# Kernel optimization log

Hardware: AMD Instinct MI355X
Metric: run time of the kernel (lower is better)

Reference implementation:

```python
import jax, jax.numpy as jnp
import numpy as np

TAU = 2.0       # LIF time constant
ALPHA = 4.0     # spikingjelly Sigmoid surrogate alpha
EPS = 1e-5      # BatchNorm eps
NUM_HEADS = 8

@jax.custom_vjp
def _spike(x):
    return (x >= 0.0).astype(x.dtype)

def _spike_fwd(x):
    return _spike(x), x

def _spike_bwd(x, g):
    s = jax.nn.sigmoid(ALPHA * x)
    return (g * ALPHA * s * (1.0 - s),)

_spike.defvjp(_spike_fwd, _spike_bwd)

def lif(x, v_th=1.0):
    """Multi-step LIF over leading time axis. v <- v + (x - v)/tau; hard reset to 0.
    detach_reset=True: spike in reset path is stop-gradient'ed."""
    def step(v, xt):
        v = v + (xt - v) / TAU
        s = _spike(v - v_th)
        v = v * (1.0 - jax.lax.stop_gradient(s))
        return v, s
    _, out = jax.lax.scan(step, jnp.zeros_like(x[0]), x)
    return out

def conv_bn(x, w, gamma, beta, mean, var, bias=None):
    """1x1 Conv1d over channel dim + BatchNorm1d (inference-style, running stats).
    x: [T,B,C,N], w: [Cout,Cin]."""
    y = jnp.einsum('tbcn,dc->tbdn', x, w)
    if bias is not None:
        y = y + bias[None, None, :, None]
    inv = gamma * jax.lax.rsqrt(var + EPS)
    return (y - mean[None, None, :, None]) * inv[None, None, :, None] + beta[None, None, :, None]

def _bn_params(key, C):
    k1, k2, k3 = jax.random.split(key, 3)
    gamma = 1.0 + 0.1 * jax.random.normal(k1, (C,), jnp.float32)
    beta = 0.1 * jax.random.normal(k2, (C,), jnp.float32)
    mean = 0.1 * jax.random.normal(k3, (C,), jnp.float32)
    var = jnp.ones((C,), jnp.float32)
    return gamma, beta, mean, var

def setup_inputs() -> dict:
    key = jax.random.key(0)
    ks = jax.random.split(key, 10)
    T, B, C, N = 4, 8, 512, 1024
    scale = 1.0 / np.sqrt(C)
    d = {}
    d['q'] = jax.random.normal(ks[0], (T, B, C, N), jnp.float32)
    d['k'] = jax.random.normal(ks[1], (T, B, C, N), jnp.float32)
    d['q_w'] = jax.random.normal(ks[2], (C, C), jnp.float32) * scale
    d['k_w'] = jax.random.normal(ks[3], (C, C), jnp.float32) * scale
    d['proj_w'] = jax.random.normal(ks[4], (C, C), jnp.float32) * scale
    d['proj_b'] = 0.01 * jax.random.normal(ks[5], (C,), jnp.float32)
    d['q_gamma'], d['q_beta'], d['q_mean'], d['q_var'] = _bn_params(ks[6], C)
    d['k_gamma'], d['k_beta'], d['k_mean'], d['k_var'] = _bn_params(ks[7], C)
    d['proj_gamma'], d['proj_beta'], d['proj_mean'], d['proj_var'] = _bn_params(ks[8], C)
    return d

def reference(q, k, q_w, k_w, proj_w, proj_b,
              q_gamma, q_beta, q_mean, q_var,
              k_gamma, k_beta, k_mean, k_var,
              proj_gamma, proj_beta, proj_mean, proj_var):
    T, B, C, N = q.shape
    H = NUM_HEADS
    Dh = C // H
    # Q path: conv1x1 + BN + LIF spikes, split heads
    q_s = lif(conv_bn(q, q_w, q_gamma, q_beta, q_mean, q_var))          # [T,B,C,N]
    q_h = q_s.reshape(T, B, H, Dh, N)
    # K path
    k_s = lif(conv_bn(k, k_w, k_gamma, k_beta, k_mean, k_var))          # [T,B,C,N]
    k_h = k_s.reshape(T, B, H, Dh, N)
    # Sum-pool Q over head_dim, spike-gate (threshold 0.5), multiply into K
    q_sum = jnp.sum(q_h, axis=3, keepdims=True)                         # [T,B,H,1,N]
    attn = lif(q_sum, v_th=0.5)                                         # [T,B,H,1,N]
    x = (attn * k_h).reshape(T, B, C, N)
    # Projection: conv1x1 (with bias) + BN + LIF
    x = conv_bn(x, proj_w, proj_gamma, proj_beta, proj_mean, proj_var, bias=proj_b)
    return lif(x)
```

## Files before the change

kernel.cpp:

```cpp
#include <hip/hip_runtime.h>
#include <hip/hip_fp16.h>
#include <stdint.h>

#define TT 4
#define BB 8
#define CC 512
#define NN 1024
#define HH 8

typedef unsigned char u8;
typedef _Float16 f16x8 __attribute__((ext_vector_type(8)));
typedef float f32x16 __attribute__((ext_vector_type(16)));

#define WF_BYTES ((size_t)2*64*512*16)
#define SZ_SPIKE ((size_t)TT*BB*CC*NN)
#define SZ_GATE  ((size_t)TT*BB*HH*NN)

union U4H { uint4 u; f16x8 v; };
__device__ __forceinline__ f16x8 ash(uint4 u){ U4H x; x.u = u; return x.v; }

#define MFMA_F16(a,b,c) __builtin_amdgcn_mfma_f32_32x32x16_f16((a),(b),(c),0,0,0)

__device__ __forceinline__ void gld_lds4(const void* g, void* l){
  __builtin_amdgcn_global_load_lds((const __attribute__((address_space(1))) void*)g,
                                   (__attribute__((address_space(3))) void*)l, 4, 0, 0);
}

#define WAITVM(N) asm volatile("s_waitcnt vmcnt(" #N ")" ::: "memory")
#define WAITLGKM0 asm volatile("s_waitcnt lgkmcnt(0)" ::: "memory")
#define SBAR() __builtin_amdgcn_s_barrier()
#define VMFENCE() asm volatile("" ::: "memory")

__device__ __forceinline__ void split16(float xs, uint32_t& h, uint32_t& m){
  __half hh = __float2half(xs);
  float hf = __half2float(hh);
  __half mm = __float2half(xs - hf);
  h = __half_as_ushort(hh);
  m = __half_as_ushort(mm);
}

__global__ __launch_bounds__(256)
void k_prep(const float* __restrict__ W0, const float* __restrict__ W1,
            const float* __restrict__ W2,
            u8* __restrict__ D0, u8* __restrict__ D1, u8* __restrict__ D2)
{
  const int which = blockIdx.y;
  const float* W = (which == 0) ? W0 : (which == 1) ? W1 : W2;
  u8* D = (which == 0) ? D0 : (which == 1) ? D1 : D2;
  const int tg  = blockIdx.x * 256 + threadIdx.x;
  const int row = tg >> 6;
  const int kh  = tg & 63;
  uint32_t Hw[4], Mw[4];
#pragma unroll
  for (int p = 0; p < 4; ++p){
    uint32_t h0, m0, h1, m1;
    split16(W[row * CC + kh * 8 + 2*p    ] * 64.0f, h0, m0);
    split16(W[row * CC + kh * 8 + 2*p + 1] * 64.0f, h1, m1);
    Hw[p] = h0 | (h1 << 16);
    Mw[p] = m0 | (m1 << 16);
  }
  *(uint4*)(D + ((size_t)(0*64 + kh)*512 + row) * 16) = make_uint4(Hw[0],Hw[1],Hw[2],Hw[3]);
  *(uint4*)(D + ((size_t)(1*64 + kh)*512 + row) * 16) = make_uint4(Mw[0],Mw[1],Mw[2],Mw[3]);
}

__global__ __launch_bounds__(256, 1)
void k_qk(const float* __restrict__ Q, const float* __restrict__ K,
          const u8* __restrict__ WFq, const u8* __restrict__ WFk,
          const float* __restrict__ qg, const float* __restrict__ qb,
          const float* __restrict__ qm, const float* __restrict__ qv,
          const float* __restrict__ kg, const float* __restrict__ kb,
          const float* __restrict__ km, const float* __restrict__ kv,
          u8* __restrict__ Sk, u8* __restrict__ Aa)
{
  __shared__ uint4 frag[2][1024];

  const int hw = blockIdx.x;
  const int lg = (hw & 7) * 64 + (hw >> 3);
  const int n0i  = lg & 31;
  const int b    = (lg >> 5) & 7;
  const int path = (lg >> 8) & 1;
  const int n0 = n0i << 5;
  const float* X = path ? K : Q;
  const u8* WF = path ? WFk : WFq;

  const int tid = threadIdx.x, lane = tid & 63, wid = tid >> 6;
  const int hi = lane >> 5, ln31 = lane & 31;

  const int c  = tid & 127;
  const int kq = tid >> 7;
  const int ct_t = c >> 5, nn = c & 31;
  const float* Xb = X + ((size_t)(ct_t*BB + b)*CC)*NN + n0 + nn;

  f32x16 acc[4][4];
#pragma unroll
  for (int i = 0; i < 4; ++i)
#pragma unroll
    for (int j = 0; j < 4; ++j)
#pragma unroll
      for (int r = 0; r < 16; ++r) acc[i][j][r] = 0.0f;

  uint4 A[16];
  float xb[2][16];

  auto loadA = [&](int H){
#pragma unroll
    for (int s = 0; s < 2; ++s)
#pragma unroll
      for (int ks = 0; ks < 2; ++ks)
#pragma unroll
        for (int rt = 0; rt < 4; ++rt)
          A[(s*2 + ks)*4 + rt] = *(const uint4*)(WF +
              ((size_t)(s*64 + H*4 + ks*2 + hi)*512
               + wid*128 + rt*32 + ln31) * 16);
  };
  auto loadX = [&](int ktile, float* xr){
    const float* xp = Xb + (size_t)(ktile*32 + kq*16)*NN;
#pragma unroll
    for (int j = 0; j < 16; ++j) xr[j] = xp[(size_t)j*NN];
  };
  auto split_write = [&](const float* xr, int fb){
    uint32_t hw_[8], mw_[8];
#pragma unroll
    for (int p = 0; p < 8; ++p){
      uint32_t ha, ma, hb2, mb2;
      split16(xr[2*p    ] * 512.0f, ha, ma);
      split16(xr[2*p + 1] * 512.0f, hb2, mb2);
      hw_[p] = ha | (hb2 << 16);
      mw_[p] = ma | (mb2 << 16);
    }
    frag[fb][(kq*2    )*128 + c] = make_uint4(hw_[0],hw_[1],hw_[2],hw_[3]);
    frag[fb][(kq*2 + 1)*128 + c] = make_uint4(hw_[4],hw_[5],hw_[6],hw_[7]);
    frag[fb][(4 + kq*2    )*128 + c] = make_uint4(mw_[0],mw_[1],mw_[2],mw_[3]);
    frag[fb][(4 + kq*2 + 1)*128 + c] = make_uint4(mw_[4],mw_[5],mw_[6],mw_[7]);
  };
  auto mstep = [&](int fb){
#pragma unroll
    for (int ks = 0; ks < 2; ++ks){
      const int kbi = ks*2 + hi;
#pragma unroll
      for (int ct = 0; ct < 4; ++ct){
        f16x8 bh = ash(frag[fb][kbi*128 + ct*32 + ln31]);
        f16x8 bm = ash(frag[fb][(4 + kbi)*128 + ct*32 + ln31]);
#pragma unroll
        for (int rt = 0; rt < 4; ++rt){
          acc[ct][rt] = MFMA_F16(ash(A[(0*2 + ks)*4 + rt]), bh, acc[ct][rt]);
          acc[ct][rt] = MFMA_F16(ash(A[(1*2 + ks)*4 + rt]), bh, acc[ct][rt]);
          acc[ct][rt] = MFMA_F16(ash(A[(0*2 + ks)*4 + rt]), bm, acc[ct][rt]);
        }
      }
    }
  };

#define QK_PH(H, XL, XN, FC, FN) { \
    loadA(H); VMFENCE(); \
    loadX((H)+2, xb[XN]); VMFENCE(); \
    split_write(xb[XL], FN); \
    mstep(FC); \
    WAITLGKM0; SBAR(); }

  loadX(0, xb[0]); VMFENCE();
  loadX(1, xb[1]); VMFENCE();
  split_write(xb[0], 0);
  WAITLGKM0; SBAR();

  for (int Hb = 0; Hb < 14; Hb += 2){
    QK_PH(Hb,     1, 0, 0, 1)
    QK_PH(Hb + 1, 0, 1, 1, 0)
  }
  { loadA(14); VMFENCE(); split_write(xb[1], 1); mstep(0); WAITLGKM0; SBAR(); }
  { loadA(15); VMFENCE(); mstep(1); }
#undef QK_PH

  const float* gamma = path ? kg : qg;
  const float* beta  = path ? kb : qb;
  const float* mean  = path ? km : qm;
  const float* var   = path ? kv : qv;

  uint32_t orb[2] = {0, 0};
#pragma unroll
  for (int rt = 0; rt < 4; ++rt)
#pragma unroll
    for (int rg = 0; rg < 4; ++rg){
      const int dbase = wid*128 + rt*32 + rg*8 + hi*4;
      const float4 g4 = *(const float4*)&gamma[dbase];
      const float4 b4 = *(const float4*)&beta[dbase];
      const float4 m4 = *(const float4*)&mean[dbase];
      const float4 v4 = *(const float4*)&var[dbase];
      const float* gp = (const float*)&g4;
      const float* bp = (const float*)&b4;
      const float* mp = (const float*)&m4;
      const float* vp = (const float*)&v4;
#pragma unroll
      for (int j = 0; j < 4; ++j){
        const float inv = gp[j] * (1.0f / sqrtf(vp[j] + 1e-5f));
        const float c1 = inv * (1.0f/32768.0f);
        const float c0 = bp[j] - mp[j]*inv;
        const int r = rg*4 + j;
        float v = 0.f;
#pragma unroll
        for (int t = 0; t < 4; ++t){
          const float y = fmaf(acc[t][rt][r], c1, c0);
          v = 0.5f*(v + y);
          const bool s = (v >= 1.0f);
          if (s) v = 0.f;
          if (path == 1)
            Sk[((size_t)(t*BB + b)*CC + dbase + j)*NN + n0 + ln31] = (u8)s;
          else
            orb[rt >> 1] |= ((uint32_t)s) << t;
        }
      }
    }

  if (path == 0){
    orb[0] |= __shfl_xor(orb[0], 32);
    orb[1] |= __shfl_xor(orb[1], 32);
    if (hi == 0){
#pragma unroll
      for (int hh = 0; hh < 2; ++hh)
#pragma unroll
        for (int t = 0; t < 4; ++t)
          Aa[((size_t)(t*BB + b)*HH + wid*2 + hh)*NN + n0 + ln31] =
              (u8)((orb[hh] >> t) & 1);
    }
  }
}

__global__ __launch_bounds__(256, 2)
void k_proj(const u8* __restrict__ Sk, const u8* __restrict__ Ag,
            const u8* __restrict__ WF, const float* __restrict__ bias,
            const float* __restrict__ gamma, const float* __restrict__ beta,
            const float* __restrict__ mean, const float* __restrict__ var,
            float* __restrict__ O)
{
  __shared__ u8   xu[3][8192];
  __shared__ uint4 frag[1024];

  const int hw = blockIdx.x;
  const int lg = (hw & 7) * 64 + (hw >> 3);
  const int d0t = lg & 1;
  const int n0i = (lg >> 1) & 31;
  const int b   = (lg >> 6) & 7;
  const int n0 = n0i << 5, d0 = d0t << 8;

  const int tid = threadIdx.x, lane = tid & 63, wid = tid >> 6;
  const int hi = lane >> 5, ln31 = lane & 31;

  const int st_kh = tid >> 5, st_t = (tid >> 3) & 3, st_n4 = tid & 7;

  f32x16 acc[4][2];
#pragma unroll
  for (int t = 0; t < 4; ++t)
#pragma unroll
    for (int rt = 0; rt < 2; ++rt)
#pragma unroll
      for (int r = 0; r < 16; ++r) acc[t][rt][r] = 0.0f;

  uint4 Ap[16];
  uint32_t gword[8];
#pragma unroll
  for (int p = 0; p < 8; ++p)
    gword[p] = *(const uint32_t*)(Ag +
        ((size_t)(st_t*BB + b)*HH + p)*NN + n0 + st_n4*4);

  auto xustage = [&](int h, int buf){
#pragma unroll
    for (int i = 0; i < 8; ++i){
      const u8* g = Sk + ((size_t)((wid*BB + b)*CC) + (size_t)(h*64 + i*8 + (lane >> 3)))*NN
                       + n0 + (lane & 7)*4;
      gld_lds4(g, (void*)&xu[buf][(wid*64 + i*8)*32]);
    }
  };
  auto loadPA = [&](int p){
#pragma unroll
    for (int s = 0; s < 2; ++s)
#pragma unroll
      for (int ks = 0; ks < 4; ++ks)
#pragma unroll
        for (int rt = 0; rt < 2; ++rt)
          Ap[(s*4 + ks)*2 + rt] = *(const uint4*)(WF +
              ((size_t)(s*64 + p*8 + ks*2 + hi)*512
               + d0 + wid*64 + rt*32 + ln31) * 16);
  };
  auto stage2 = [&](int buf, uint32_t g32){
    uint32_t r[8];
#pragma unroll
    for (int cc = 0; cc < 8; ++cc)
      r[cc] = *(const uint32_t*)&xu[buf][(st_t*64 + st_kh*8 + cc)*32 + st_n4*4];
#pragma unroll
    for (int j = 0; j < 4; ++j){
      const uint32_t gm   = __builtin_amdgcn_perm(g32, g32, (uint32_t)j * 0x01010101u);
      const uint32_t selp = (uint32_t)j | (((uint32_t)j + 4u) << 8);
      uint32_t p01 = __builtin_amdgcn_perm(r[1], r[0], selp);
      uint32_t p23 = __builtin_amdgcn_perm(r[3], r[2], selp);
      uint32_t p45 = __builtin_amdgcn_perm(r[5], r[4], selp);
      uint32_t p67 = __builtin_amdgcn_perm(r[7], r[6], selp);
      uint32_t lo  = __builtin_amdgcn_perm(p23, p01, 0x05040100u) & gm;
      uint32_t hi_ = __builtin_amdgcn_perm(p67, p45, 0x05040100u) & gm;
      uint32_t w[4];
#pragma unroll
      for (int p = 0; p < 4; ++p){
        const uint32_t src = (p < 2) ? lo : hi_;
        const uint32_t b0 = (src >> ((p & 1) * 16)) & 0xFFu;
        const uint32_t b1 = (src >> ((p & 1) * 16 + 8)) & 0xFFu;
        w[p] = (b0 ? 0x3C00u : 0u) | (b1 ? 0x3C000000u : 0u);
      }
      frag[st_kh*128 + st_t*32 + st_n4*4 + j] = make_uint4(w[0], w[1], w[2], w[3]);
    }
  };
  auto mstepP = [&](){
#pragma unroll
    for (int ks = 0; ks < 4; ++ks){
      const int kbi = ks*2 + hi;
#pragma unroll
      for (int ct = 0; ct < 4; ++ct){
        const int fb = ct*32 + ln31;
        f16x8 bb = ash(frag[kbi*128 + fb]);
#pragma unroll
        for (int rt = 0; rt < 2; ++rt){
          acc[ct][rt] = MFMA_F16(ash(Ap[(0*4 + ks)*2 + rt]), bb, acc[ct][rt]);
          acc[ct][rt] = MFMA_F16(ash(Ap[(1*4 + ks)*2 + rt]), bb, acc[ct][rt]);
        }
      }
    }
  };

#define PJ_PH(P, VM) { \
    WAITVM(VM); SBAR(); \
    loadPA(P); VMFENCE(); \
    if ((P) < 6) { xustage((P)+2, ((P)+2)%3); VMFENCE(); } \
    stage2((P)%3, gword[P]); \
    WAITLGKM0; SBAR(); \
    mstepP(); }

  xustage(0, 0); VMFENCE(); xustage(1, 1); VMFENCE();
  PJ_PH(0,8) PJ_PH(1,8) PJ_PH(2,8) PJ_PH(3,8)
  PJ_PH(4,8) PJ_PH(5,8) PJ_PH(6,8) PJ_PH(7,0)
#undef PJ_PH

#pragma unroll
  for (int rt = 0; rt < 2; ++rt)
#pragma unroll
    for (int rg = 0; rg < 4; ++rg){
      const int dbase = d0 + wid*64 + rt*32 + rg*8 + hi*4;
      const float4 g4 = *(const float4*)&gamma[dbase];
      const float4 b4 = *(const float4*)&beta[dbase];
      const float4 m4 = *(const float4*)&mean[dbase];
      const float4 v4 = *(const float4*)&var[dbase];
      const float4 s4 = *(const float4*)&bias[dbase];
      const float* gp = (const float*)&g4;
      const float* bp = (const float*)&b4;
      const float* mp = (const float*)&m4;
      const float* vp = (const float*)&v4;
      const float* sp = (const float*)&s4;
#pragma unroll
      for (int j = 0; j < 4; ++j){
        const float inv = gp[j] * (1.0f / sqrtf(vp[j] + 1e-5f));
        const float c1 = inv * (1.0f/64.0f);
        const float c0 = (sp[j] - mp[j])*inv + bp[j];
        const int r = rg*4 + j;
        float v = 0.f;
#pragma unroll
        for (int t = 0; t < 4; ++t){
          const float y = fmaf(acc[t][rt][r], c1, c0);
          v = 0.5f*(v + y);
          const bool s = (v >= 1.0f);
          if (s) v = 0.f;
          O[((size_t)(t*BB + b)*CC + dbase + j)*NN + n0 + ln31] = s ? 1.f : 0.f;
        }
      }
    }
}

extern "C" void kernel_launch(void* const* d_in, const int* in_sizes, int n_in,
                              void* d_out, int out_size, void* d_ws, size_t ws_size,
                              hipStream_t stream)
{
  const float* q   = (const float*)d_in[0];
  const float* k   = (const float*)d_in[1];
  const float* qw  = (const float*)d_in[2];
  const float* kw  = (const float*)d_in[3];
  const float* pw  = (const float*)d_in[4];
  const float* pb  = (const float*)d_in[5];
  const float* qg  = (const float*)d_in[6];
  const float* qbt = (const float*)d_in[7];
  const float* qm  = (const float*)d_in[8];
  const float* qv  = (const float*)d_in[9];
  const float* kg  = (const float*)d_in[10];
  const float* kbt = (const float*)d_in[11];
  const float* km  = (const float*)d_in[12];
  const float* kv  = (const float*)d_in[13];
  const float* pg  = (const float*)d_in[14];
  const float* pbt = (const float*)d_in[15];
  const float* pm  = (const float*)d_in[16];
  const float* pv  = (const float*)d_in[17];

  u8* WFq = (u8*)d_ws;
  u8* WFk = WFq + WF_BYTES;
  u8* WFp = WFk + WF_BYTES;
  u8* Sk  = WFp + WF_BYTES;
  u8* Aa  = Sk + SZ_SPIKE;
  const size_t need = 3*WF_BYTES + SZ_SPIKE + SZ_GATE;
  if (ws_size < need) return;

  k_prep<<<dim3(128, 3), 256, 0, stream>>>(qw, kw, pw, WFq, WFk, WFp);
  k_qk<<<512, 256, 0, stream>>>(q, k, WFq, WFk,
                                qg, qbt, qm, qv, kg, kbt, km, kv, Sk, Aa);
  k_proj<<<512, 256, 0, stream>>>(Sk, Aa, WFp, pb, pg, pbt, pm, pv, (float*)d_out);
}
```

Measured before the change: 182.2 us.

## Pre-split inputs into fp16 hi/lo panels and stream them via async LDS loads

Adds a separate kernel that converts the fp32 Q and K activations into pre-laid-out fp16 high/low fragment panels in workspace. The QK GEMM then loads these panels straight into a three-stage LDS ring with global_load_lds and double-buffers the weight fragments in registers. This takes the per-element conversion and strided global loads out of the GEMM main loop. In exchange, the full activation tensors are written to and re-read from memory in the same byte count, which adds a lot of DRAM traffic and an extra launch.

```diff
diff --git a/kernel.cpp b/kernel.cpp
--- a/kernel.cpp
+++ b/kernel.cpp
@@ -13,6 +13,7 @@
 typedef float f32x16 __attribute__((ext_vector_type(16)));
 
 #define WF_BYTES ((size_t)2*64*512*16)
+#define XF_BYTES ((size_t)8*32*262144)
 #define SZ_SPIKE ((size_t)TT*BB*CC*NN)
 #define SZ_GATE  ((size_t)TT*BB*HH*NN)
 
@@ -21,6 +22,10 @@
 
 #define MFMA_F16(a,b,c) __builtin_amdgcn_mfma_f32_32x32x16_f16((a),(b),(c),0,0,0)
 
+__device__ __forceinline__ void gld_lds16(const void* g, void* l){
+  __builtin_amdgcn_global_load_lds((const __attribute__((address_space(1))) void*)g,
+                                   (__attribute__((address_space(3))) void*)l, 16, 0, 0);
+}
 __device__ __forceinline__ void gld_lds4(const void* g, void* l){
   __builtin_amdgcn_global_load_lds((const __attribute__((address_space(1))) void*)g,
                                    (__attribute__((address_space(3))) void*)l, 4, 0, 0);
@@ -63,8 +68,46 @@
   *(uint4*)(D + ((size_t)(1*64 + kh)*512 + row) * 16) = make_uint4(Mw[0],Mw[1],Mw[2],Mw[3]);
 }
 
+__global__ __launch_bounds__(256)
+void k_splitx(const float* __restrict__ Q, const float* __restrict__ K,
+              u8* __restrict__ XFq, u8* __restrict__ XFk)
+{
+  const int z = blockIdx.z;
+  const float* X = (z < 32) ? Q : K;
+  u8* XF = (z < 32) ? XFq : XFk;
+  const int tb = z & 31, t = tb >> 3, b = tb & 7;
+  const int n4 = threadIdx.x & 63, khl = threadIdx.x >> 6;
+  const int kh = blockIdx.y * 4 + khl;
+  const int n  = blockIdx.x * 256 + n4 * 4;
+  const float* xp = X + ((size_t)((t*BB + b)*CC) + (size_t)kh*8)*NN + n;
+  float4 xv[8];
+#pragma unroll
+  for (int p = 0; p < 8; ++p) xv[p] = *(const float4*)(xp + (size_t)p * NN);
+
+  u8* panel = XF + ((size_t)(b*32 + (n >> 5)) << 18);
+  const int colb = t*32 + (n & 31);
+#pragma unroll
+  for (int jj = 0; jj < 4; ++jj){
+    uint32_t Hw[4], Mw[4];
+#pragma unroll
+    for (int wi = 0; wi < 4; ++wi){
+      const float* f0 = (const float*)&xv[2*wi];
+      const float* f1 = (const float*)&xv[2*wi + 1];
+      uint32_t h0, m0, h1, m1;
+      split16(f0[jj] * 512.0f, h0, m0);
+      split16(f1[jj] * 512.0f, h1, m1);
+      Hw[wi] = h0 | (h1 << 16);
+      Mw[wi] = m0 | (m1 << 16);
+    }
+    *(uint4*)(panel + ((size_t)((0*64 + kh)*128 + colb + jj))*16) =
+        make_uint4(Hw[0],Hw[1],Hw[2],Hw[3]);
+    *(uint4*)(panel + ((size_t)((1*64 + kh)*128 + colb + jj))*16) =
+        make_uint4(Mw[0],Mw[1],Mw[2],Mw[3]);
+  }
+}
+
 __global__ __launch_bounds__(256, 1)
-void k_qk(const float* __restrict__ Q, const float* __restrict__ K,
+void k_qk(const u8* __restrict__ XFq, const u8* __restrict__ XFk,
           const u8* __restrict__ WFq, const u8* __restrict__ WFk,
           const float* __restrict__ qg, const float* __restrict__ qb,
           const float* __restrict__ qm, const float* __restrict__ qv,
@@ -72,7 +115,7 @@
           const float* __restrict__ km, const float* __restrict__ kv,
           u8* __restrict__ Sk, u8* __restrict__ Aa)
 {
-  __shared__ uint4 frag[2][1024];
+  __shared__ uint4 ring[3][1024];
 
   const int hw = blockIdx.x;
   const int lg = (hw & 7) * 64 + (hw >> 3);
@@ -80,16 +123,12 @@
   const int b    = (lg >> 5) & 7;
   const int path = (lg >> 8) & 1;
   const int n0 = n0i << 5;
-  const float* X = path ? K : Q;
+  const u8* XF = path ? XFk : XFq;
   const u8* WF = path ? WFk : WFq;
 
   const int tid = threadIdx.x, lane = tid & 63, wid = tid >> 6;
   const int hi = lane >> 5, ln31 = lane & 31;
-
-  const int c  = tid & 127;
-  const int kq = tid >> 7;
-  const int ct_t = c >> 5, nn = c & 31;
-  const float* Xb = X + ((size_t)(ct_t*BB + b)*CC)*NN + n0 + nn;
+  const u8* panel = XF + ((size_t)(b*32 + n0i) << 18);
 
   f32x16 acc[4][4];
 #pragma unroll
@@ -99,77 +138,66 @@
 #pragma unroll
       for (int r = 0; r < 16; ++r) acc[i][j][r] = 0.0f;
 
-  uint4 A[16];
-  float xb[2][16];
-
-  auto loadA = [&](int H){
-#pragma unroll
-    for (int s = 0; s < 2; ++s)
-#pragma unroll
-      for (int ks = 0; ks < 2; ++ks)
-#pragma unroll
-        for (int rt = 0; rt < 4; ++rt)
-          A[(s*2 + ks)*4 + rt] = *(const uint4*)(WF +
-              ((size_t)(s*64 + H*4 + ks*2 + hi)*512
-               + wid*128 + rt*32 + ln31) * 16);
-  };
-  auto loadX = [&](int ktile, float* xr){
-    const float* xp = Xb + (size_t)(ktile*32 + kq*16)*NN;
-#pragma unroll
-    for (int j = 0; j < 16; ++j) xr[j] = xp[(size_t)j*NN];
-  };
-  auto split_write = [&](const float* xr, int fb){
-    uint32_t hw_[8], mw_[8];
-#pragma unroll
-    for (int p = 0; p < 8; ++p){
-      uint32_t ha, ma, hb2, mb2;
-      split16(xr[2*p    ] * 512.0f, ha, ma);
-      split16(xr[2*p + 1] * 512.0f, hb2, mb2);
-      hw_[p] = ha | (hb2 << 16);
-      mw_[p] = ma | (mb2 << 16);
-    }
-    frag[fb][(kq*2    )*128 + c] = make_uint4(hw_[0],hw_[1],hw_[2],hw_[3]);
-    frag[fb][(kq*2 + 1)*128 + c] = make_uint4(hw_[4],hw_[5],hw_[6],hw_[7]);
-    frag[fb][(4 + kq*2    )*128 + c] = make_uint4(mw_[0],mw_[1],mw_[2],mw_[3]);
-    frag[fb][(4 + kq*2 + 1)*128 + c] = make_uint4(mw_[4],mw_[5],mw_[6],mw_[7]);
-  };
-  auto mstep = [&](int fb){
-#pragma unroll
-    for (int ks = 0; ks < 2; ++ks){
-      const int kbi = ks*2 + hi;
+  uint4 A0[16], A1[16];
+
+  auto stage = [&](int t, int buf){
+#pragma unroll
+    for (int i = 0; i < 4; ++i){
+      const int c = wid*4 + i;
+      const int s = c >> 3, kl = (c & 7) >> 1, half = c & 1;
+      const u8* g = panel + ((size_t)((s*64 + t*4 + kl)*128 + half*64 + lane)) * 16;
+      gld_lds16(g, (void*)&ring[buf][(s*4 + kl)*128 + half*64]);
+    }
+  };
+  auto loadA = [&](int t, uint4* A){
+#pragma unroll
+    for (int q2 = 0; q2 < 4; ++q2){
+      const int s16h = q2 >> 1, s = q2 & 1;
+#pragma unroll
+      for (int rt = 0; rt < 4; ++rt)
+        A[q2*4 + rt] = *(const uint4*)(WF +
+            ((size_t)(s*64 + t*4 + s16h*2 + hi)*512
+             + wid*128 + rt*32 + ln31) * 16);
+    }
+  };
+  auto mstep = [&](const uint4* A, int buf){
+#pragma unroll
+    for (int s16h = 0; s16h < 2; ++s16h){
+      const int klr = s16h*2 + hi;
 #pragma unroll
       for (int ct = 0; ct < 4; ++ct){
-        f16x8 bh = ash(frag[fb][kbi*128 + ct*32 + ln31]);
-        f16x8 bm = ash(frag[fb][(4 + kbi)*128 + ct*32 + ln31]);
+        f16x8 bh = ash(ring[buf][(0*4 + klr)*128 + ct*32 + ln31]);
+        f16x8 bm = ash(ring[buf][(1*4 + klr)*128 + ct*32 + ln31]);
 #pragma unroll
         for (int rt = 0; rt < 4; ++rt){
-          acc[ct][rt] = MFMA_F16(ash(A[(0*2 + ks)*4 + rt]), bh, acc[ct][rt]);
-          acc[ct][rt] = MFMA_F16(ash(A[(1*2 + ks)*4 + rt]), bh, acc[ct][rt]);
-          acc[ct][rt] = MFMA_F16(ash(A[(0*2 + ks)*4 + rt]), bm, acc[ct][rt]);
+          acc[ct][rt] = MFMA_F16(ash(A[(s16h*2+0)*4+rt]), bh, acc[ct][rt]);
+          acc[ct][rt] = MFMA_F16(ash(A[(s16h*2+1)*4+rt]), bh, acc[ct][rt]);
+          acc[ct][rt] = MFMA_F16(ash(A[(s16h*2+0)*4+rt]), bm, acc[ct][rt]);
         }
       }
     }
   };
 
-#define QK_PH(H, XL, XN, FC, FN) { \
-    loadA(H); VMFENCE(); \
-    loadX((H)+2, xb[XN]); VMFENCE(); \
-    split_write(xb[XL], FN); \
-    mstep(FC); \
-    WAITLGKM0; SBAR(); }
-
-  loadX(0, xb[0]); VMFENCE();
-  loadX(1, xb[1]); VMFENCE();
-  split_write(xb[0], 0);
-  WAITLGKM0; SBAR();
-
-  for (int Hb = 0; Hb < 14; Hb += 2){
-    QK_PH(Hb,     1, 0, 0, 1)
-    QK_PH(Hb + 1, 0, 1, 1, 0)
-  }
-  { loadA(14); VMFENCE(); split_write(xb[1], 1); mstep(0); WAITLGKM0; SBAR(); }
-  { loadA(15); VMFENCE(); mstep(1); }
-#undef QK_PH
+  stage(0, 0); VMFENCE();
+  loadA(0, A0); VMFENCE();
+  stage(1, 1); VMFENCE();
+
+#define QK_IT(T, AC, AN) { \
+    WAITVM(4); WAITLGKM0; SBAR(); \
+    loadA((T)+1, AN); VMFENCE(); \
+    if ((T) < 14) { stage((T)+2, ((T)+2)%3); VMFENCE(); } \
+    mstep(AC, (T)%3); }
+
+  QK_IT(0,  A0, A1)  QK_IT(1,  A1, A0)
+  QK_IT(2,  A0, A1)  QK_IT(3,  A1, A0)
+  QK_IT(4,  A0, A1)  QK_IT(5,  A1, A0)
+  QK_IT(6,  A0, A1)  QK_IT(7,  A1, A0)
+  QK_IT(8,  A0, A1)  QK_IT(9,  A1, A0)
+  QK_IT(10, A0, A1)  QK_IT(11, A1, A0)
+  QK_IT(12, A0, A1)  QK_IT(13, A1, A0)
+  QK_IT(14, A0, A1)
+  { WAITVM(0); WAITLGKM0; SBAR(); mstep(A1, 15%3); }
+#undef QK_IT
 
   const float* gamma = path ? kg : qg;
   const float* beta  = path ? kb : qb;
@@ -397,13 +425,16 @@
   u8* WFq = (u8*)d_ws;
   u8* WFk = WFq + WF_BYTES;
   u8* WFp = WFk + WF_BYTES;
-  u8* Sk  = WFp + WF_BYTES;
+  u8* XFq = WFp + WF_BYTES;
+  u8* XFk = XFq + XF_BYTES;
+  u8* Sk  = XFk + XF_BYTES;
   u8* Aa  = Sk + SZ_SPIKE;
-  const size_t need = 3*WF_BYTES + SZ_SPIKE + SZ_GATE;
+  const size_t need = 3*WF_BYTES + 2*XF_BYTES + SZ_SPIKE + SZ_GATE;
   if (ws_size < need) return;
 
   k_prep<<<dim3(128, 3), 256, 0, stream>>>(qw, kw, pw, WFq, WFk, WFp);
-  k_qk<<<512, 256, 0, stream>>>(q, k, WFq, WFk,
+  k_splitx<<<dim3(4, 16, 64), 256, 0, stream>>>(q, k, XFq, XFk);
+  k_qk<<<512, 256, 0, stream>>>(XFq, XFk, WFq, WFk,
                                 qg, qbt, qm, qv, kg, kbt, km, kv, Sk, Aa);
   k_proj<<<512, 256, 0, stream>>>(Sk, Aa, WFp, pb, pg, pbt, pm, pv, (float*)d_out);
 }
```

Result: slower. 253.8 us (+39.3%).
